# Performance work log

Measured on AMD Instinct MI355X. Metric: run time of the kernel, lower is better.

Reference implementation:

```python
import jax, jax.numpy as jnp
import numpy as np

# ---- configuration (matches init_kwargs) ----
B, C_IO, T = 2, 64, 4096
PATCH = 2
W0, W1 = 512, 1024           # widths
D_DN, D_MID = 2, 4           # depths per level
DH = 64                      # dim per head
WIN = 128                    # local attention window
MAP = 1024                   # mapping_dim
DFF_MAP = 1024               # mapping_d_ff
FF_MULT = 2                  # GEGLU ff_mult in local levels
H_DN = W0 // DH              # 8 heads
H_MID = W1 // DH             # 16 heads


def _n(key, shape, s=0.02):
    return jax.random.normal(key, shape, jnp.float32) * s


def setup_inputs() -> dict:
    key = jax.random.key(0)
    ks = iter(jax.random.split(key, 64))
    p = {}
    p['x'] = jax.random.normal(next(ks), (B, C_IO, T), jnp.float32)
    p['t'] = jax.random.uniform(next(ks), (B,), jnp.float32)
    p['time_w'] = jax.random.normal(next(ks), (MAP // 2, 1), jnp.float32)
    p['time_in_w'] = _n(next(ks), (MAP, MAP))
    p['map_in_s'] = jnp.ones((MAP,), jnp.float32)
    p['map_norm_s'] = jnp.ones((2, MAP), jnp.float32)
    p['map_up_w'] = _n(next(ks), (2, MAP, 2 * DFF_MAP))
    p['map_down_w'] = _n(next(ks), (2, DFF_MAP, MAP))
    p['map_out_s'] = jnp.ones((MAP,), jnp.float32)
    p['patch_in_w'] = _n(next(ks), (C_IO * PATCH, W0))
    p['dn_anorm_w'] = _n(next(ks), (D_DN, MAP, W0))
    p['dn_qkv_w'] = _n(next(ks), (D_DN, W0, 3 * W0))
    p['dn_o_w'] = _n(next(ks), (D_DN, W0, W0))
    p['dn_fnorm_w'] = _n(next(ks), (D_DN, MAP, W0))
    p['dn_ff1_w'] = _n(next(ks), (D_DN, W0, 2 * FF_MULT * W0))
    p['dn_ff2_w'] = _n(next(ks), (D_DN, FF_MULT * W0, W0))
    p['merge_w'] = _n(next(ks), (W0 * 2, W1))
    p['mid_map_w'] = _n(next(ks), (MAP, W1))
    p['mid_pin_w'] = _n(next(ks), (W1, W1))
    p['mid_pout_w'] = _n(next(ks), (W1, W1))
    p['mid_ln1_g'] = jnp.ones((D_MID, W1), jnp.float32)
    p['mid_ln1_b'] = jnp.zeros((D_MID, W1), jnp.float32)
    p['mid_qkv_w'] = _n(next(ks), (D_MID, W1, 3 * W1))
    p['mid_o_w'] = _n(next(ks), (D_MID, W1, W1))
    p['mid_ln2_g'] = jnp.ones((D_MID, W1), jnp.float32)
    p['mid_ln2_b'] = jnp.zeros((D_MID, W1), jnp.float32)
    p['mid_ff1_w'] = _n(next(ks), (D_MID, W1, 8 * W1))
    p['mid_ff2_w'] = _n(next(ks), (D_MID, 4 * W1, W1))
    p['mid_fn_g'] = jnp.ones((W1,), jnp.float32)
    p['mid_fn_b'] = jnp.zeros((W1,), jnp.float32)
    p['split_w'] = _n(next(ks), (W1, W0 * 2))
    p['split_fac'] = jnp.full((1,), 0.5, jnp.float32)
    p['up_anorm_w'] = _n(next(ks), (D_DN, MAP, W0))
    p['up_qkv_w'] = _n(next(ks), (D_DN, W0, 3 * W0))
    p['up_o_w'] = _n(next(ks), (D_DN, W0, W0))
    p['up_fnorm_w'] = _n(next(ks), (D_DN, MAP, W0))
    p['up_ff1_w'] = _n(next(ks), (D_DN, W0, 2 * FF_MULT * W0))
    p['up_ff2_w'] = _n(next(ks), (D_DN, FF_MULT * W0, W0))
    p['out_norm_s'] = jnp.ones((W0,), jnp.float32)
    p['patch_out_w'] = _n(next(ks), (W0, C_IO * PATCH))
    return p


def rmsnorm(x, scale, eps=1e-6):
    ms = jnp.mean(jnp.square(x), -1, keepdims=True)
    return x * (scale * jax.lax.rsqrt(ms + eps))


def layernorm(x, g, b, eps=1e-5):
    m = jnp.mean(x, -1, keepdims=True)
    v = jnp.mean(jnp.square(x - m), -1, keepdims=True)
    return (x - m) * jax.lax.rsqrt(v + eps) * g + b


def rope_tables(S, D):
    inv = 1.0 / (10000.0 ** (jnp.arange(0, D, 2, dtype=jnp.float32) / D))
    ang = jnp.arange(S, dtype=jnp.float32)[:, None] * inv  # [S, D/2]
    return jnp.cos(ang), jnp.sin(ang)


def apply_rope(x, cos, sin):
    # x: [B,H,S,D], contiguous-half rotation
    x1, x2 = jnp.split(x, 2, -1)
    return jnp.concatenate([x1 * cos - x2 * sin, x2 * cos + x1 * sin], -1)


def heads_split(x, h):
    Bx, S, C = x.shape
    return x.reshape(Bx, S, h, C // h).transpose(0, 2, 1, 3)


def heads_merge(x):
    Bx, h, S, D = x.shape
    return x.transpose(0, 2, 1, 3).reshape(Bx, S, h * D)


def local_attn(q, k, v, w):
    # non-causal sliding-window attention: each query window attends to
    # [prev, self, next] windows (look_backward=1, look_forward=1)
    Bx, H, S, D = q.shape
    nw = S // w
    qw = q.reshape(Bx, H, nw, w, D)
    def ctx(tn):
        tw = tn.reshape(Bx, H, nw, w, D)
        pad = jnp.pad(tw, ((0, 0), (0, 0), (1, 1), (0, 0), (0, 0)))
        return jnp.concatenate([pad[:, :, :-2], pad[:, :, 1:-1], pad[:, :, 2:]], 3)  # [B,H,nw,3w,D]
    kw, vw = ctx(k), ctx(v)
    s = jnp.einsum('bhnqd,bhnkd->bhnqk', qw * (D ** -0.5), kw)
    valid = jnp.ones((nw, 3 * w), bool).at[0, :w].set(False).at[-1, 2 * w:].set(False)
    s = jnp.where(valid[None, None, :, None, :], s, jnp.finfo(s.dtype).min)
    a = jax.nn.softmax(s, -1)
    return jnp.einsum('bhnqk,bhnkd->bhnqd', a, vw).reshape(Bx, H, S, D)


def token_merge(x, w, r=2):
    # 'b (n r) c -> b n (c r)' then linear
    Bx, S, C = x.shape
    x = x.reshape(Bx, S // r, r, C).transpose(0, 1, 3, 2).reshape(Bx, S // r, C * r)
    return x @ w


def token_split(x, w, r=2):
    # linear then 'b n (c r) -> b (n r) c'
    y = x @ w
    Bx, n, CR = y.shape
    C = CR // r
    return y.reshape(Bx, n, C, r).transpose(0, 1, 3, 2).reshape(Bx, n * r, C)


def mapping(e, in_s, norm_s, up_w, down_w, out_s):
    x = rmsnorm(e, in_s)
    for l in range(up_w.shape[0]):
        h = rmsnorm(x, norm_s[l])
        a, g = jnp.split(h @ up_w[l], 2, -1)
        x = x + (a * jax.nn.gelu(g)) @ down_w[l]
    return rmsnorm(x, out_s)


def local_level(x, cond, anorm, qkv_w, o_w, fnorm, ff1, ff2, heads, win):
    Bx, S, C = x.shape
    D = C // heads
    cos, sin = rope_tables(S, D)
    for l in range(qkv_w.shape[0]):
        h = rmsnorm(x, 1.0 + (cond @ anorm[l])[:, None, :])  # AdaRMSNorm
        q, k, v = jnp.split(h @ qkv_w[l], 3, -1)
        q, k, v = heads_split(q, heads), heads_split(k, heads), heads_split(v, heads)
        q, k = apply_rope(q, cos, sin), apply_rope(k, cos, sin)
        x = x + heads_merge(local_attn(q, k, v, win)) @ o_w[l]
        h = rmsnorm(x, 1.0 + (cond @ fnorm[l])[:, None, :])
        a, g = jnp.split(h @ ff1[l], 2, -1)
        x = x + (a * jax.nn.gelu(g)) @ ff2[l]  # GEGLU FF
    return x


def mid_level(x, ln1g, ln1b, qkv_w, o_w, ln2g, ln2b, ff1, ff2, fng, fnb, heads):
    Bx, S, C = x.shape
    D = C // heads
    cos, sin = rope_tables(S, D)
    for l in range(qkv_w.shape[0]):
        h = layernorm(x, ln1g[l], ln1b[l])
        q, k, v = jnp.split(h @ qkv_w[l], 3, -1)
        q, k, v = heads_split(q, heads), heads_split(k, heads), heads_split(v, heads)
        q, k = apply_rope(q, cos, sin), apply_rope(k, cos, sin)
        s = jnp.einsum('bhqd,bhkd->bhqk', q * (D ** -0.5), k)
        o = jnp.einsum('bhqk,bhkd->bhqd', jax.nn.softmax(s, -1), v)
        x = x + heads_merge(o) @ o_w[l]
        h = layernorm(x, ln2g[l], ln2b[l])
        a, g = jnp.split(h @ ff1[l], 2, -1)
        x = x + (a * jax.nn.silu(g)) @ ff2[l]  # SwiGLU FF
    return layernorm(x, fng, fnb)


def _forward(x, t, time_w, time_in_w, map_in_s, map_norm_s, map_up_w, map_down_w, map_out_s,
             patch_in_w, dn_anorm_w, dn_qkv_w, dn_o_w, dn_fnorm_w, dn_ff1_w, dn_ff2_w,
             merge_w, mid_map_w, mid_pin_w, mid_pout_w, mid_ln1_g, mid_ln1_b, mid_qkv_w,
             mid_o_w, mid_ln2_g, mid_ln2_b, mid_ff1_w, mid_ff2_w, mid_fn_g, mid_fn_b,
             split_w, split_fac, up_anorm_w, up_qkv_w, up_o_w, up_fnorm_w, up_ff1_w,
             up_ff2_w, out_norm_s, patch_out_w):
    h = jnp.swapaxes(x, 1, 2)                      # [B,T,C_io]
    h = token_merge(h, patch_in_w, PATCH)          # [B, T/2, W0]
    f = 2.0 * jnp.pi * (t[:, None] @ time_w.T)     # Fourier features
    temb = jnp.concatenate([jnp.cos(f), jnp.sin(f)], -1) @ time_in_w
    cond = mapping(temb, map_in_s, map_norm_s, map_up_w, map_down_w, map_out_s)  # [B,MAP]
    h = local_level(h, cond, dn_anorm_w, dn_qkv_w, dn_o_w, dn_fnorm_w, dn_ff1_w, dn_ff2_w, H_DN, WIN)
    skip = h
    h = token_merge(h, merge_w)                    # [B, T/4, W1]
    h = h @ mid_pin_w
    pre = (cond @ mid_map_w)[:, None, :]           # prepended mapping token
    h = jnp.concatenate([pre, h], 1)
    h = mid_level(h, mid_ln1_g, mid_ln1_b, mid_qkv_w, mid_o_w, mid_ln2_g, mid_ln2_b,
                  mid_ff1_w, mid_ff2_w, mid_fn_g, mid_fn_b, H_MID)
    h = (h @ mid_pout_w)[:, 1:, :]
    h = token_split(h, split_w)                    # back to [B, T/2, W0]
    h = skip + split_fac * (h - skip)              # lerp skip fusion
    h = local_level(h, cond, up_anorm_w, up_qkv_w, up_o_w, up_fnorm_w, up_ff1_w, up_ff2_w, H_DN, WIN)
    h = rmsnorm(h, out_norm_s)
    h = token_split(h, patch_out_w, PATCH)         # [B,T,C_io]
    return jnp.swapaxes(h, 1, 2)


def reference(x, t, time_w, time_in_w, map_in_s, map_norm_s, map_up_w, map_down_w, map_out_s,
              patch_in_w, dn_anorm_w, dn_qkv_w, dn_o_w, dn_fnorm_w, dn_ff1_w, dn_ff2_w,
              merge_w, mid_map_w, mid_pin_w, mid_pout_w, mid_ln1_g, mid_ln1_b, mid_qkv_w,
              mid_o_w, mid_ln2_g, mid_ln2_b, mid_ff1_w, mid_ff2_w, mid_fn_g, mid_fn_b,
              split_w, split_fac, up_anorm_w, up_qkv_w, up_o_w, up_fnorm_w, up_ff1_w,
              up_ff2_w, out_norm_s, patch_out_w):
    return _forward(x, t, time_w, time_in_w, map_in_s, map_norm_s, map_up_w, map_down_w, map_out_s,
                    patch_in_w, dn_anorm_w, dn_qkv_w, dn_o_w, dn_fnorm_w, dn_ff1_w, dn_ff2_w,
                    merge_w, mid_map_w, mid_pin_w, mid_pout_w, mid_ln1_g, mid_ln1_b, mid_qkv_w,
                    mid_o_w, mid_ln2_g, mid_ln2_b, mid_ff1_w, mid_ff2_w, mid_fn_g, mid_fn_b,
                    split_w, split_fac, up_anorm_w, up_qkv_w, up_o_w, up_fnorm_w, up_ff1_w,
                    up_ff2_w, out_norm_s, patch_out_w)
```

## Files before the change

kernel.cpp:

```cpp
#include <hip/hip_runtime.h>
#include <math.h>

#define BB   2
#define CIO  64
#define TT   4096
#define S0   2048
#define W0   512
#define HDN  8
#define SM   1025
#define SMP  1088
#define W1   1024
#define HMID 16
#define WIN  128
#define NW   16
#define MAPD 1024
#define KSPL 16
#define PKCAP 8396800L

typedef _Float16 f16;
typedef _Float16 half8 __attribute__((ext_vector_type(8)));
typedef _Float16 half4v __attribute__((ext_vector_type(4)));
typedef _Float16 half2v __attribute__((ext_vector_type(2)));
typedef float floatx4 __attribute__((ext_vector_type(4)));

__device__ __forceinline__ float gelu_tanh(float x) {
    float x3 = x * x * x;
    return 0.5f * x * (1.f + tanhf(0.7978845608028654f * (x + 0.044715f * x3)));
}

__global__ __launch_bounds__(256) void wcast(
    const float* __restrict__ W, f16* __restrict__ Wt, int K, int N) {
    __shared__ float T[64][65];
    const int n0 = blockIdx.x * 64, k0 = blockIdx.y * 64;
    const int tid = threadIdx.x;
    for (int e = tid; e < 4096; e += 256) {
        int r = e >> 6, c = e & 63;
        T[r][c] = W[(size_t)(k0 + r) * N + n0 + c];
    }
    __syncthreads();
    for (int e = tid; e < 2048; e += 256) {
        int r = e >> 5, c2 = (e & 31) * 2;
        half2v p;
        p[0] = (f16)T[c2][r];
        p[1] = (f16)T[c2 + 1][r];
        *(half2v*)(Wt + (size_t)(n0 + r) * K + k0 + c2) = p;
    }
}

template<int OUTM>
__global__ __launch_bounds__(256) void gemm_h(
    const f16* __restrict__ A, const f16* __restrict__ Bt,
    const float* __restrict__ res, void* __restrict__ Cv,
    int M, int N, int K) {
    __shared__ __align__(16) f16 As[2][4096];
    __shared__ __align__(16) f16 Bs[2][4096];
    const int tid = threadIdx.x;
    const int wv = tid >> 6, ln = tid & 63;
    int nwg = gridDim.x * gridDim.y;
    int orig = blockIdx.y * gridDim.x + blockIdx.x;
    int wg = orig;
    if (nwg >= 16) {
        int q = nwg >> 3, r = nwg & 7;
        int xcd = orig & 7, lot = orig >> 3;
        wg = (xcd < r ? xcd * (q + 1) : r * (q + 1) + (xcd - r) * q) + lot;
    }
    const int bm = (wg / gridDim.x) * 128, bn = (wg % gridDim.x) * 128;
    int Kc = K, kbase = 0;
    if (OUTM == 2) { Kc = K / gridDim.z; kbase = blockIdx.z * Kc; }
    const int nt = Kc >> 5;

    auto stage = [&](int buf, int kt) {
        int k0 = kbase + (kt << 5);
#pragma unroll
        for (int i = 0; i < 2; ++i) {
            int off = i * 4096 + wv * 1024 + ln * 16;
            int row = off >> 6, kb = (off & 63) >> 1;
            int gr = bm + row; gr = gr < M ? gr : M - 1;
            f16* gp = const_cast<f16*>(A) + (size_t)gr * K + k0 + kb;
            __builtin_amdgcn_global_load_lds(
                (__attribute__((address_space(1))) void*)gp,
                (__attribute__((address_space(3))) void*)(&As[buf][i * 2048 + wv * 512]),
                16, 0, 0);
            f16* gq = const_cast<f16*>(Bt) + (size_t)(bn + row) * K + k0 + kb;
            __builtin_amdgcn_global_load_lds(
                (__attribute__((address_space(1))) void*)gq,
                (__attribute__((address_space(3))) void*)(&Bs[buf][i * 2048 + wv * 512]),
                16, 0, 0);
        }
    };

    floatx4 acc[4][4];
#pragma unroll
    for (int m = 0; m < 4; ++m)
#pragma unroll
        for (int n = 0; n < 4; ++n) acc[m][n] = (floatx4)0.f;
    const int r = ln & 15, kc = (ln >> 4) * 8;
    const int wr = (wv >> 1) * 64, wc = (wv & 1) * 64;

    stage(0, 0);
    for (int t = 0; t < nt; ++t) {
        __syncthreads();
        if (t + 1 < nt) stage((t + 1) & 1, t + 1);
        const int buf = t & 1;
        half8 af[4], bf[4];
#pragma unroll
        for (int m = 0; m < 4; ++m)
            af[m] = *(const half8*)(&As[buf][(wr + m * 16 + r) * 32 + kc]);
#pragma unroll
        for (int n = 0; n < 4; ++n)
            bf[n] = *(const half8*)(&Bs[buf][(wc + n * 16 + r) * 32 + kc]);
#pragma unroll
        for (int m = 0; m < 4; ++m)
#pragma unroll
            for (int n = 0; n < 4; ++n)
                acc[m][n] = __builtin_amdgcn_mfma_f32_16x16x32_f16(af[m], bf[n], acc[m][n], 0, 0, 0);
    }

    float* Cf = (float*)Cv;
    f16*   Ch = (f16*)Cv;
    if (OUTM == 2) Cf += (size_t)blockIdx.z * M * N;
#pragma unroll
    for (int m = 0; m < 4; ++m) {
        int rbase = bm + wr + m * 16 + ((ln >> 4) << 2);
#pragma unroll
        for (int j = 0; j < 4; ++j) {
            int row = rbase + j;
            if (row < M) {
                size_t ro = (size_t)row * N;
#pragma unroll
                for (int n = 0; n < 4; ++n) {
                    int col = bn + wc + n * 16 + (ln & 15);
                    float v = acc[m][n][j];
                    if (OUTM == 1) Ch[ro + col] = (f16)v;
                    else if (OUTM == 0) Cf[ro + col] = v + (res ? res[ro + col] : 0.f);
                    else Cf[ro + col] = v;
                }
            }
        }
    }
}

template<bool HOUT>
__global__ __launch_bounds__(256) void kred(
    const float* __restrict__ P, const float* __restrict__ res,
    void* __restrict__ Cv, size_t mn, int ks) {
    size_t i = ((size_t)blockIdx.x * 256 + threadIdx.x) * 4;
    if (i >= mn) return;
    floatx4 s = res ? *(const floatx4*)(res + i) : (floatx4)0.f;
    for (int z = 0; z < ks; ++z) {
        floatx4 p = *(const floatx4*)(P + (size_t)z * mn + i);
        s += p;
    }
    if (HOUT) {
        half4v h;
#pragma unroll
        for (int j = 0; j < 4; ++j) h[j] = (f16)s[j];
        *(half4v*)((f16*)Cv + i) = h;
    } else {
        *(floatx4*)((float*)Cv + i) = s;
    }
}

__global__ __launch_bounds__(256) void gemv2_part(
    const float* __restrict__ A, const float* __restrict__ W,
    float* __restrict__ P, int N, int K) {
    int n = blockIdx.x * 256 + threadIdx.x;
    if (n >= N) return;
    int Kc = K / KSPL;
    int k0 = blockIdx.y * Kc;
    float acc0 = 0.f, acc1 = 0.f;
    const float* Wp = W + (size_t)k0 * N + n;
    const float* a0 = A + k0;
    const float* a1 = A + K + k0;
#pragma unroll 4
    for (int k = 0; k < Kc; ++k) {
        float w = Wp[(size_t)k * N];
        acc0 = fmaf(a0[k], w, acc0);
        acc1 = fmaf(a1[k], w, acc1);
    }
    P[((size_t)blockIdx.y * 2 + 0) * N + n] = acc0;
    P[((size_t)blockIdx.y * 2 + 1) * N + n] = acc1;
}

__global__ __launch_bounds__(256) void gemv2_red(
    const float* __restrict__ P, const float* __restrict__ res,
    float* __restrict__ C, int N) {
    int g = blockIdx.x * 256 + threadIdx.x;
    if (g >= 2 * N) return;
    int m = g / N, n = g - m * N;
    float s = res ? res[g] : 0.f;
#pragma unroll
    for (int ky = 0; ky < KSPL; ++ky)
        s += P[((size_t)ky * 2 + m) * N + n];
    C[g] = s;
}

__device__ __forceinline__ void stf(float* p, float v) { *p = v; }
__device__ __forceinline__ void stf(f16* p, float v)   { *p = (f16)v; }

template<typename TO>
__global__ __launch_bounds__(256) void rmsnorm_k(
    const float* __restrict__ X, const float* __restrict__ scale,
    TO* __restrict__ Y, int C, int rows_per_group, float sadd) {
    int row = blockIdx.x, tid = threadIdx.x;
    const float* x = X + (size_t)row * C;
    float v[8];
    int cnt = C >> 8;
    float ss = 0.f;
    for (int i = 0; i < cnt; ++i) { v[i] = x[tid + (i << 8)]; ss += v[i] * v[i]; }
    __shared__ float red[256];
    red[tid] = ss; __syncthreads();
    for (int s2 = 128; s2; s2 >>= 1) { if (tid < s2) red[tid] += red[tid + s2]; __syncthreads(); }
    float inv = rsqrtf(red[0] / (float)C + 1e-6f);
    const float* sc = scale + (size_t)(row / rows_per_group) * C;
    TO* y = Y + (size_t)row * C;
    for (int i = 0; i < cnt; ++i) {
        int c = tid + (i << 8);
        stf(&y[c], v[i] * (sadd + sc[c]) * inv);
    }
}

__global__ __launch_bounds__(256) void layernorm_k(
    const float* __restrict__ X, const float* __restrict__ g,
    const float* __restrict__ bta, f16* __restrict__ Y, int C) {
    int row = blockIdx.x, tid = threadIdx.x;
    const float* x = X + (size_t)row * C;
    float v[8];
    int cnt = C >> 8;
    float s = 0.f;
    for (int i = 0; i < cnt; ++i) { v[i] = x[tid + (i << 8)]; s += v[i]; }
    __shared__ float red[256];
    red[tid] = s; __syncthreads();
    for (int s2 = 128; s2; s2 >>= 1) { if (tid < s2) red[tid] += red[tid + s2]; __syncthreads(); }
    float m = red[0] / (float)C;
    __syncthreads();
    float s2s = 0.f;
    for (int i = 0; i < cnt; ++i) { float d = v[i] - m; s2s += d * d; }
    red[tid] = s2s; __syncthreads();
    for (int s2 = 128; s2; s2 >>= 1) { if (tid < s2) red[tid] += red[tid + s2]; __syncthreads(); }
    float inv = rsqrtf(red[0] / (float)C + 1e-5f);
    f16* y = Y + (size_t)row * C;
    for (int i = 0; i < cnt; ++i) {
        int c = tid + (i << 8);
        y[c] = (f16)((v[i] - m) * inv * g[c] + bta[c]);
    }
}

__global__ __launch_bounds__(256) void glu_k(
    const float* __restrict__ U, float* __restrict__ Yo,
    size_t total, int F, int mode) {
    size_t gidx = (size_t)blockIdx.x * 256 + threadIdx.x;
    if (gidx >= total) return;
    size_t r = gidx / (size_t)F;
    int c = (int)(gidx - r * F);
    const float* u = U + r * (size_t)(2 * F);
    float a = u[c], gg = u[F + c];
    float act = (mode == 0) ? gelu_tanh(gg) : gg / (1.f + expf(-gg));
    Yo[gidx] = a * act;
}

__global__ __launch_bounds__(256) void glu_h8(
    const f16* __restrict__ U, f16* __restrict__ Yo,
    size_t total8, int F8, int mode) {
    size_t gi = (size_t)blockIdx.x * 256 + threadIdx.x;
    if (gi >= total8) return;
    size_t r = gi / (size_t)F8;
    int c = (int)(gi - r * (size_t)F8);
    const f16* u = U + r * (size_t)F8 * 16;
    half8 av = *(const half8*)(u + c * 8);
    half8 gv = *(const half8*)(u + F8 * 8 + c * 8);
    half8 y;
#pragma unroll
    for (int j = 0; j < 8; ++j) {
        float a = (float)av[j], gg = (float)gv[j];
        float act = (mode == 0) ? gelu_tanh(gg) : gg / (1.f + __expf(-gg));
        y[j] = (f16)(a * act);
    }
    *(half8*)(Yo + gi * 8) = y;
}

__global__ __launch_bounds__(256) void qkv_split_rope(
    const float* __restrict__ QKV, f16* __restrict__ Qo,
    f16* __restrict__ Ko, f16* __restrict__ Vo, int S, int H) {
    int g = blockIdx.x * 256 + threadIdx.x;
    int total = BB * S * H * 32;
    if (g >= total) return;
    int i = g & 31;
    int tix = g >> 5;
    int h = tix % H; tix /= H;
    int s = tix % S; int b = tix / S;
    int C = H * 64;
    const float* base = QKV + (size_t)(b * S + s) * 3 * C + h * 64;
    float q1 = base[i], q2 = base[32 + i];
    float k1 = base[C + i], k2 = base[C + 32 + i];
    float v1 = base[2 * C + i], v2 = base[2 * C + 32 + i];
    float inv = expf(-(float)i * 0.28782313662425575f);
    float ang = (float)s * inv;
    float sn, cs;
    sincosf(ang, &sn, &cs);
    size_t o = ((size_t)(b * H + h) * S + s) * 64 + i;
    Qo[o]      = (f16)((q1 * cs - q2 * sn) * 0.125f);
    Qo[o + 32] = (f16)((q2 * cs + q1 * sn) * 0.125f);
    Ko[o]      = (f16)(k1 * cs - k2 * sn);
    Ko[o + 32] = (f16)(k2 * cs + k1 * sn);
    Vo[o]      = (f16)v1;
    Vo[o + 32] = (f16)v2;
}

__global__ __launch_bounds__(256) void vtrans(
    const f16* __restrict__ V, f16* __restrict__ Vt, int S, int Spad) {
    __shared__ f16 T[64][72];
    const int tid = threadIdx.x;
    const int k0 = blockIdx.x * 64;
    const f16* Vb = V + (size_t)blockIdx.y * S * 64;
    f16* Vtb = Vt + (size_t)blockIdx.y * 64 * Spad;
    for (int c = tid; c < 512; c += 256) {
        int kk = c >> 3, d8 = (c & 7) * 8;
        int kg = k0 + kk; kg = kg < S ? kg : S - 1;
        half8 v = *(const half8*)(Vb + (size_t)kg * 64 + d8);
        if (k0 + kk >= S) {
#pragma unroll
            for (int j = 0; j < 8; ++j) v[j] = (f16)0.f;
        }
        *(half8*)(&T[kk][d8]) = v;
    }
    __syncthreads();
    for (int c = tid; c < 512; c += 256) {
        int d = c >> 3, k8 = (c & 7) * 8;
        half8 o;
#pragma unroll
        for (int j = 0; j < 8; ++j) o[j] = T[k8 + j][d];
        *(half8*)(Vtb + (size_t)d * Spad + k0 + k8) = o;
    }
}

__global__ __launch_bounds__(256) void fattn(
    const f16* __restrict__ Q, const f16* __restrict__ K,
    const f16* __restrict__ Vt, f16* __restrict__ O,
    int S, int Spad, int H, int win) {
    __shared__ __align__(16) f16 Ks[64][72];
    __shared__ __align__(16) f16 Vs[64][72];
    __shared__ __align__(16) f16 Ps[4][32][72];
    const int tid = threadIdx.x;
    const int wv = tid >> 6, ln = tid & 63;
    const int r15 = ln & 15, g = ln >> 4;
    const int bh = blockIdx.y;
    const int b = bh / H, h = bh % H;
    const int q0 = (int)blockIdx.x * 128;
    const f16* Qb = Q + (size_t)bh * S * 64;
    const f16* Kb = K + (size_t)bh * S * 64;
    const f16* Vtb = Vt + (size_t)bh * 64 * Spad;

    half8 aq[2][2];
#pragma unroll
    for (int m = 0; m < 2; ++m) {
        int q = q0 + wv * 32 + m * 16 + r15;
        q = q < S ? q : S - 1;
#pragma unroll
        for (int ks = 0; ks < 2; ++ks)
            aq[m][ks] = *(const half8*)(Qb + (size_t)q * 64 + ks * 32 + g * 8);
    }
    floatx4 o[2][4];
#pragma unroll
    for (int m = 0; m < 2; ++m)
#pragma unroll
        for (int n = 0; n < 4; ++n) o[m][n] = (floatx4)0.f;
    float mst[2][4], lst[2][4];
#pragma unroll
    for (int m = 0; m < 2; ++m)
#pragma unroll
        for (int j = 0; j < 4; ++j) { mst[m][j] = -3.0e38f; lst[m][j] = 0.f; }

    int klo = 0, khi = S;
    if (win) {
        int n = (int)blockIdx.x;
        klo = (n - 1) * win; if (klo < 0) klo = 0;
        khi = (n + 2) * win; if (khi > S) khi = S;
    }
    for (int kb = klo; kb < khi; kb += 64) {
        __syncthreads();
#pragma unroll
        for (int i = 0; i < 2; ++i) {
            int c = tid + i * 256;
            int rr = c >> 3, c8 = (c & 7) * 8;
            int kg = kb + rr; kg = kg < S ? kg : S - 1;
            *(half8*)(&Ks[rr][c8]) = *(const half8*)(Kb + (size_t)kg * 64 + c8);
            *(half8*)(&Vs[rr][c8]) = *(const half8*)(Vtb + (size_t)rr * Spad + kb + c8);
        }
        __syncthreads();
        floatx4 s[2][4];
#pragma unroll
        for (int m = 0; m < 2; ++m)
#pragma unroll
            for (int n = 0; n < 4; ++n) s[m][n] = (floatx4)0.f;
#pragma unroll
        for (int ks = 0; ks < 2; ++ks) {
            half8 bk[4];
#pragma unroll
            for (int n = 0; n < 4; ++n)
                bk[n] = *(const half8*)(&Ks[n * 16 + r15][ks * 32 + g * 8]);
#pragma unroll
            for (int m = 0; m < 2; ++m)
#pragma unroll
                for (int n = 0; n < 4; ++n)
                    s[m][n] = __builtin_amdgcn_mfma_f32_16x16x32_f16(aq[m][ks], bk[n], s[m][n], 0, 0, 0);
        }
        if (kb + 64 > S) {
#pragma unroll
            for (int n = 0; n < 4; ++n)
                if (kb + n * 16 + r15 >= S) {
#pragma unroll
                    for (int m = 0; m < 2; ++m) s[m][n] = (floatx4)(-3.0e38f);
                }
        }
#pragma unroll
        for (int m = 0; m < 2; ++m) {
#pragma unroll
            for (int j = 0; j < 4; ++j) {
                float tm = fmaxf(fmaxf(s[m][0][j], s[m][1][j]), fmaxf(s[m][2][j], s[m][3][j]));
                tm = fmaxf(tm, __shfl_xor(tm, 1));
                tm = fmaxf(tm, __shfl_xor(tm, 2));
                tm = fmaxf(tm, __shfl_xor(tm, 4));
                tm = fmaxf(tm, __shfl_xor(tm, 8));
                float mn = fmaxf(mst[m][j], tm);
                float sc = __expf(mst[m][j] - mn);
                mst[m][j] = mn;
                float ts = 0.f;
#pragma unroll
                for (int n = 0; n < 4; ++n) {
                    float p = __expf(s[m][n][j] - mn);
                    s[m][n][j] = p;
                    ts += p;
                }
                ts += __shfl_xor(ts, 1);
                ts += __shfl_xor(ts, 2);
                ts += __shfl_xor(ts, 4);
                ts += __shfl_xor(ts, 8);
                lst[m][j] = lst[m][j] * sc + ts;
#pragma unroll
                for (int n = 0; n < 4; ++n) o[m][n][j] *= sc;
            }
        }
#pragma unroll
        for (int m = 0; m < 2; ++m)
#pragma unroll
            for (int n = 0; n < 4; ++n)
#pragma unroll
                for (int j = 0; j < 4; ++j)
                    Ps[wv][m * 16 + g * 4 + j][n * 16 + r15] = (f16)s[m][n][j];
#pragma unroll
        for (int ks = 0; ks < 2; ++ks) {
            half8 pa[2], bv[4];
#pragma unroll
            for (int m = 0; m < 2; ++m)
                pa[m] = *(const half8*)(&Ps[wv][m * 16 + r15][ks * 32 + g * 8]);
#pragma unroll
            for (int n = 0; n < 4; ++n)
                bv[n] = *(const half8*)(&Vs[n * 16 + r15][ks * 32 + g * 8]);
#pragma unroll
            for (int m = 0; m < 2; ++m)
#pragma unroll
                for (int n = 0; n < 4; ++n)
                    o[m][n] = __builtin_amdgcn_mfma_f32_16x16x32_f16(pa[m], bv[n], o[m][n], 0, 0, 0);
        }
    }
    const int HC = H * 64;
#pragma unroll
    for (int m = 0; m < 2; ++m)
#pragma unroll
        for (int j = 0; j < 4; ++j) {
            int q = q0 + wv * 32 + m * 16 + g * 4 + j;
            if (q < S) {
                float inv = 1.f / lst[m][j];
                size_t ro = ((size_t)b * S + q) * HC + h * 64;
#pragma unroll
                for (int n = 0; n < 4; ++n)
                    O[ro + n * 16 + r15] = (f16)(o[m][n][j] * inv);
            }
        }
}

__global__ __launch_bounds__(256) void patch_in_gather(
    const float* __restrict__ x, f16* __restrict__ out) {
    int g = blockIdx.x * 256 + threadIdx.x;
    if (g >= BB * S0 * 128) return;
    int k = g & 127;
    int n = (g >> 7) & (S0 - 1);
    int b = g >> 18;
    out[g] = (f16)x[(size_t)b * CIO * TT + (size_t)(k >> 1) * TT + 2 * n + (k & 1)];
}

__global__ __launch_bounds__(256) void time_embed(
    const float* __restrict__ t, const float* __restrict__ tw,
    float* __restrict__ te) {
    int g = blockIdx.x * 256 + threadIdx.x;
    if (g >= BB * MAPD) return;
    int b = g / MAPD, j = g % MAPD;
    float w = tw[(j < 512) ? j : j - 512];
    float ang = 6.283185307179586f * t[b] * w;
    te[g] = (j < 512) ? cosf(ang) : sinf(ang);
}

__global__ __launch_bounds__(256) void token_merge_gather(
    const float* __restrict__ A, f16* __restrict__ out) {
    int g = blockIdx.x * 256 + threadIdx.x;
    if (g >= BB * 1024 * 1024) return;
    int k = g & 1023;
    int n = (g >> 10) & 1023;
    int b = g >> 20;
    out[g] = (f16)A[((size_t)b * S0 + 2 * n + (k & 1)) * W0 + (k >> 1)];
}

__global__ __launch_bounds__(256) void concat_mid(
    const float* __restrict__ pre, const float* __restrict__ Dsrc,
    float* __restrict__ Cm) {
    int g = blockIdx.x * 256 + threadIdx.x;
    if (g >= BB * SM * W1) return;
    int c = g & 1023;
    int row = g >> 10;
    int b = row / SM, r = row % SM;
    Cm[g] = (r == 0) ? pre[b * W1 + c]
                     : Dsrc[((size_t)b * 1024 + r - 1) * W1 + c];
}

__global__ __launch_bounds__(256) void gather_drop(
    const f16* __restrict__ Dsrc, f16* __restrict__ out) {
    int g = blockIdx.x * 256 + threadIdx.x;
    if (g >= BB * 1024 * W1) return;
    int c = g & 1023;
    int n = (g >> 10) & 1023;
    int b = g >> 20;
    out[g] = Dsrc[((size_t)b * SM + 1 + n) * W1 + c];
}

__global__ __launch_bounds__(256) void split_scatter_lerp(
    const float* __restrict__ y, const float* __restrict__ skip,
    const float* __restrict__ fac, float* __restrict__ xo) {
    int g = blockIdx.x * 256 + threadIdx.x;
    if (g >= BB * S0 * W0) return;
    int c = g & 511;
    int tk = (g >> 9) & (S0 - 1);
    int b = g >> 20;
    float yv = y[((size_t)b * 1024 + (tk >> 1)) * W1 + (c * 2 + (tk & 1))];
    float sk = skip[g];
    xo[g] = sk + fac[0] * (yv - sk);
}

__global__ __launch_bounds__(256) void patch_out_scatter(
    const float* __restrict__ y, float* __restrict__ out) {
    int g = blockIdx.x * 256 + threadIdx.x;
    if (g >= BB * CIO * TT) return;
    int tk = g & (TT - 1);
    int c = (g >> 12) & 63;
    int b = g >> 18;
    out[g] = y[((size_t)b * S0 + (tk >> 1)) * 128 + (c * 2 + (tk & 1))];
}

extern "C" void kernel_launch(void* const* d_in, const int* in_sizes, int n_in,
                              void* d_out, int out_size, void* d_ws, size_t ws_size,
                              hipStream_t stream) {
    const float* x          = (const float*)d_in[0];
    const float* t          = (const float*)d_in[1];
    const float* time_w     = (const float*)d_in[2];
    const float* time_in_w  = (const float*)d_in[3];
    const float* map_in_s   = (const float*)d_in[4];
    const float* map_norm_s = (const float*)d_in[5];
    const float* map_up_w   = (const float*)d_in[6];
    const float* map_down_w = (const float*)d_in[7];
    const float* map_out_s  = (const float*)d_in[8];
    const float* patch_in_w = (const float*)d_in[9];
    const float* dn_anorm_w = (const float*)d_in[10];
    const float* dn_qkv_w   = (const float*)d_in[11];
    const float* dn_o_w     = (const float*)d_in[12];
    const float* dn_fnorm_w = (const float*)d_in[13];
    const float* dn_ff1_w   = (const float*)d_in[14];
    const float* dn_ff2_w   = (const float*)d_in[15];
    const float* merge_w    = (const float*)d_in[16];
    const float* mid_map_w  = (const float*)d_in[17];
    const float* mid_pin_w  = (const float*)d_in[18];
    const float* mid_pout_w = (const float*)d_in[19];
    const float* mid_ln1_g  = (const float*)d_in[20];
    const float* mid_ln1_b  = (const float*)d_in[21];
    const float* mid_qkv_w  = (const float*)d_in[22];
    const float* mid_o_w    = (const float*)d_in[23];
    const float* mid_ln2_g  = (const float*)d_in[24];
    const float* mid_ln2_b  = (const float*)d_in[25];
    const float* mid_ff1_w  = (const float*)d_in[26];
    const float* mid_ff2_w  = (const float*)d_in[27];
    const float* mid_fn_g   = (const float*)d_in[28];
    const float* mid_fn_b   = (const float*)d_in[29];
    const float* split_w    = (const float*)d_in[30];
    const float* split_fac  = (const float*)d_in[31];
    const float* up_anorm_w = (const float*)d_in[32];
    const float* up_qkv_w   = (const float*)d_in[33];
    const float* up_o_w     = (const float*)d_in[34];
    const float* up_fnorm_w = (const float*)d_in[35];
    const float* up_ff1_w   = (const float*)d_in[36];
    const float* up_ff2_w   = (const float*)d_in[37];
    const float* out_norm_s = (const float*)d_in[38];
    const float* patch_out_w= (const float*)d_in[39];

    float* Wp = (float*)d_ws;
    size_t off = 0;
    auto alloc = [&](size_t n) { float* p = Wp + off; off += n; return p; };
    float* A   = alloc((size_t)4096 * 512);
    float* Bsk = alloc((size_t)4096 * 512);
    float* Cm  = alloc((size_t)2050 * 1024);
    float* Df  = alloc((size_t)2050 * 1024);
    float* E32 = alloc((size_t)2050 * 3072);
    f16*  Fq   = (f16*)alloc((size_t)1049600);
    f16*  Fk   = (f16*)alloc((size_t)1049600);
    f16*  Fv   = (f16*)alloc((size_t)1049600);
    f16*  Fvt  = (f16*)alloc((size_t)1114112);
    f16*  H1   = (f16*)alloc((size_t)8396800);
    f16*  H2   = (f16*)alloc((size_t)4198400);
    f16*  Wh   = (f16*)alloc((size_t)4194304);
    float* Pk  = alloc((size_t)PKCAP);
    float* Pb  = alloc((size_t)KSPL * 2 * 2048);
    float* Sma = alloc((size_t)32768);
    (void)ws_size; (void)in_sizes; (void)n_in; (void)out_size;

    float* te   = Sma;
    float* temb = Sma + 2048;
    float* mapx = Sma + 4096;
    float* maph = Sma + 6144;
    float* mapu = Sma + 8192;
    float* mapg = Sma + 12288;
    float* cond = Sma + 14336;
    float* sA   = Sma + 16384;
    float* sF   = Sma + 17408;
    float* pre  = Sma + 18432;

    auto WC = [&](const float* W, int K, int N) {
        wcast<<<dim3(N / 64, K / 64), 256, 0, stream>>>(W, Wh, K, N);
    };
    auto pick_ks = [](int M, int N, int K) {
        long gx = N / 128, gy = (M + 127) / 128;
        int ks = 1;
        while (gx * gy * ks < 512 && ks < 8) {
            int nk = ks * 2;
            if ((K / nk) % 32 != 0 || (long)M * N * nk > PKCAP) break;
            ks = nk;
        }
        return ks;
    };
    auto GF = [&](const f16* Aa, const float* res, float* C, int M, int N, int K) {
        int ks = pick_ks(M, N, K);
        dim3 g(N / 128, (M + 127) / 128, ks);
        if (ks == 1) {
            gemm_h<0><<<g, 256, 0, stream>>>(Aa, Wh, res, C, M, N, K);
        } else {
            gemm_h<2><<<g, 256, 0, stream>>>(Aa, Wh, nullptr, Pk, M, N, K);
            size_t mn = (size_t)M * N;
            kred<false><<<(int)((mn / 4 + 255) / 256), 256, 0, stream>>>(Pk, res, C, mn, ks);
        }
    };
    auto GH = [&](const f16* Aa, f16* C, int M, int N, int K) {
        int ks = pick_ks(M, N, K);
        dim3 g(N / 128, (M + 127) / 128, ks);
        if (ks == 1) {
            gemm_h<1><<<g, 256, 0, stream>>>(Aa, Wh, nullptr, C, M, N, K);
        } else {
            gemm_h<2><<<g, 256, 0, stream>>>(Aa, Wh, nullptr, Pk, M, N, K);
            size_t mn = (size_t)M * N;
            kred<true><<<(int)((mn / 4 + 255) / 256), 256, 0, stream>>>(Pk, nullptr, C, mn, ks);
        }
    };
    auto gemv2 = [&](const float* Aa, const float* W, const float* res,
                     float* C, int N, int K) {
        gemv2_part<<<dim3((N + 255) / 256, KSPL), 256, 0, stream>>>(Aa, W, Pb, N, K);
        gemv2_red<<<(2 * N + 255) / 256, 256, 0, stream>>>(Pb, res, C, N);
    };

    patch_in_gather<<<(BB * S0 * 128 + 255) / 256, 256, 0, stream>>>(x, H2);
    WC(patch_in_w, 128, 512);
    GF(H2, nullptr, A, 4096, 512, 128);

    time_embed<<<(BB * MAPD + 255) / 256, 256, 0, stream>>>(t, time_w, te);
    gemv2(te, time_in_w, nullptr, temb, 1024, 1024);
    rmsnorm_k<float><<<2, 256, 0, stream>>>(temb, map_in_s, mapx, 1024, 2, 0.f);
    for (int l = 0; l < 2; ++l) {
        rmsnorm_k<float><<<2, 256, 0, stream>>>(mapx, map_norm_s + (size_t)l * 1024, maph, 1024, 2, 0.f);
        gemv2(maph, map_up_w + (size_t)l * 1024 * 2048, nullptr, mapu, 2048, 1024);
        glu_k<<<(2 * 1024 + 255) / 256, 256, 0, stream>>>(mapu, mapg, 2 * 1024, 1024, 0);
        gemv2(mapg, map_down_w + (size_t)l * 1024 * 1024, mapx, mapx, 1024, 1024);
    }
    rmsnorm_k<float><<<2, 256, 0, stream>>>(mapx, map_out_s, cond, 1024, 2, 0.f);

    auto run_local = [&](const float* anorm, const float* qkvw, const float* ow,
                         const float* fnorm, const float* ff1, const float* ff2) {
        for (int l = 0; l < 2; ++l) {
            gemv2(cond, anorm + (size_t)l * 1024 * 512, nullptr, sA, 512, 1024);
            rmsnorm_k<f16><<<4096, 256, 0, stream>>>(A, sA, H2, 512, 2048, 1.f);
            WC(qkvw + (size_t)l * 512 * 1536, 512, 1536);
            GF(H2, nullptr, E32, 4096, 1536, 512);
            qkv_split_rope<<<(BB * S0 * HDN * 32 + 255) / 256, 256, 0, stream>>>(E32, Fq, Fk, Fv, S0, HDN);
            vtrans<<<dim3(S0 / 64, BB * HDN), 256, 0, stream>>>(Fv, Fvt, S0, S0);
            fattn<<<dim3(S0 / 128, BB * HDN), 256, 0, stream>>>(Fq, Fk, Fvt, H2, S0, S0, HDN, WIN);
            WC(ow + (size_t)l * 512 * 512, 512, 512);
            GF(H2, A, A, 4096, 512, 512);
            gemv2(cond, fnorm + (size_t)l * 1024 * 512, nullptr, sF, 512, 1024);
            rmsnorm_k<f16><<<4096, 256, 0, stream>>>(A, sF, H2, 512, 2048, 1.f);
            WC(ff1 + (size_t)l * 512 * 2048, 512, 2048);
            GH(H2, H1, 4096, 2048, 512);
            glu_h8<<<(4096 * 128 + 255) / 256, 256, 0, stream>>>(H1, H2, (size_t)4096 * 128, 128, 0);
            WC(ff2 + (size_t)l * 1024 * 512, 1024, 512);
            GF(H2, A, A, 4096, 512, 1024);
        }
    };
    run_local(dn_anorm_w, dn_qkv_w, dn_o_w, dn_fnorm_w, dn_ff1_w, dn_ff2_w);

    hipMemcpyAsync(Bsk, A, (size_t)4096 * 512 * 4, hipMemcpyDeviceToDevice, stream);
    token_merge_gather<<<(BB * 1024 * 1024 + 255) / 256, 256, 0, stream>>>(A, H2);
    WC(merge_w, 1024, 1024);
    GH(H2, H1, 2048, 1024, 1024);
    WC(mid_pin_w, 1024, 1024);
    GF(H1, nullptr, Df, 2048, 1024, 1024);
    gemv2(cond, mid_map_w, nullptr, pre, 1024, 1024);
    concat_mid<<<(BB * SM * W1 + 255) / 256, 256, 0, stream>>>(pre, Df, Cm);

    for (int l = 0; l < 4; ++l) {
        layernorm_k<<<2050, 256, 0, stream>>>(Cm, mid_ln1_g + (size_t)l * 1024,
                                              mid_ln1_b + (size_t)l * 1024, H2, 1024);
        WC(mid_qkv_w + (size_t)l * 1024 * 3072, 1024, 3072);
        GF(H2, nullptr, E32, 2050, 3072, 1024);
        qkv_split_rope<<<(BB * SM * HMID * 32 + 255) / 256, 256, 0, stream>>>(E32, Fq, Fk, Fv, SM, HMID);
        vtrans<<<dim3(SMP / 64, BB * HMID), 256, 0, stream>>>(Fv, Fvt, SM, SMP);
        fattn<<<dim3(9, BB * HMID), 256, 0, stream>>>(Fq, Fk, Fvt, H2, SM, SMP, HMID, 0);
        WC(mid_o_w + (size_t)l * 1024 * 1024, 1024, 1024);
        GF(H2, Cm, Cm, 2050, 1024, 1024);
        layernorm_k<<<2050, 256, 0, stream>>>(Cm, mid_ln2_g + (size_t)l * 1024,
                                              mid_ln2_b + (size_t)l * 1024, H2, 1024);
        WC(mid_ff1_w + (size_t)l * 1024 * 8192, 1024, 8192);
        GH(H2, H1, 2050, 8192, 1024);
        glu_h8<<<(int)(((size_t)2050 * 512 + 255) / 256), 256, 0, stream>>>(H1, H2, (size_t)2050 * 512, 512, 1);
        WC(mid_ff2_w + (size_t)l * 4096 * 1024, 4096, 1024);
        GF(H2, Cm, Cm, 2050, 1024, 4096);
    }
    layernorm_k<<<2050, 256, 0, stream>>>(Cm, mid_fn_g, mid_fn_b, H2, 1024);

    WC(mid_pout_w, 1024, 1024);
    GH(H2, H1, 2050, 1024, 1024);
    gather_drop<<<(BB * 1024 * W1 + 255) / 256, 256, 0, stream>>>(H1, H2);
    WC(split_w, 1024, 1024);
    GF(H2, nullptr, Df, 2048, 1024, 1024);
    split_scatter_lerp<<<(BB * S0 * W0 + 255) / 256, 256, 0, stream>>>(Df, Bsk, split_fac, A);

    run_local(up_anorm_w, up_qkv_w, up_o_w, up_fnorm_w, up_ff1_w, up_ff2_w);

    rmsnorm_k<f16><<<4096, 256, 0, stream>>>(A, out_norm_s, H2, 512, 4096, 0.f);
    WC(patch_out_w, 512, 128);
    GF(H2, nullptr, Df, 4096, 128, 512);
    patch_out_scatter<<<(BB * CIO * TT + 255) / 256, 256, 0, stream>>>(Df, (float*)d_out);
}
```

Baseline: 2.187 ms.

## Split attention over key ranges with separate softmax-combine kernel

Adds a split-K (flash-decoding style) mode to the attention kernel: each block handles a slice of key tiles and writes unnormalized fp32 partial outputs plus running max and sum. A new combine kernel merges the partials with log-sum-exp weighting and writes fp16 output. The goal is more blocks in flight for the low-occupancy attention grids (9x32 mid, 16x16 local). The cost is extra fp32 partial traffic, an extra launch, and reuse of the Pk scratch buffer.

```diff
diff --git a/kernel.cpp b/kernel.cpp
--- a/kernel.cpp
+++ b/kernel.cpp
@@ -336,8 +336,9 @@
 
 __global__ __launch_bounds__(256) void fattn(
     const f16* __restrict__ Q, const f16* __restrict__ K,
-    const f16* __restrict__ Vt, f16* __restrict__ O,
-    int S, int Spad, int H, int win) {
+    const f16* __restrict__ Vt, float* __restrict__ Op,
+    float* __restrict__ Mst, float* __restrict__ Lst,
+    int S, int Spad, int H, int win, int QR) {
     __shared__ __align__(16) f16 Ks[64][72];
     __shared__ __align__(16) f16 Vs[64][72];
     __shared__ __align__(16) f16 Ps[4][32][72];
@@ -345,7 +346,8 @@
     const int wv = tid >> 6, ln = tid & 63;
     const int r15 = ln & 15, g = ln >> 4;
     const int bh = blockIdx.y;
-    const int b = bh / H, h = bh % H;
+    const int NBH = gridDim.y;
+    const int z = blockIdx.z, nz = gridDim.z;
     const int q0 = (int)blockIdx.x * 128;
     const f16* Qb = Q + (size_t)bh * S * 64;
     const f16* Kb = K + (size_t)bh * S * 64;
@@ -377,7 +379,12 @@
         klo = (n - 1) * win; if (klo < 0) klo = 0;
         khi = (n + 2) * win; if (khi > S) khi = S;
     }
-    for (int kb = klo; kb < khi; kb += 64) {
+    int ntile = (khi - klo + 63) >> 6;
+    int chunk = (ntile + nz - 1) / nz;
+    int myLo = klo + z * chunk * 64;
+    int myHi = klo + (z + 1) * chunk * 64; if (myHi > khi) myHi = khi;
+
+    for (int kb = myLo; kb < myHi; kb += 64) {
         __syncthreads();
 #pragma unroll
         for (int i = 0; i < 2; ++i) {
@@ -464,20 +471,51 @@
                     o[m][n] = __builtin_amdgcn_mfma_f32_16x16x32_f16(pa[m], bv[n], o[m][n], 0, 0, 0);
         }
     }
-    const int HC = H * 64;
+    size_t zb = ((size_t)z * NBH + bh) * QR;
 #pragma unroll
     for (int m = 0; m < 2; ++m)
 #pragma unroll
         for (int j = 0; j < 4; ++j) {
-            int q = q0 + wv * 32 + m * 16 + g * 4 + j;
-            if (q < S) {
-                float inv = 1.f / lst[m][j];
-                size_t ro = ((size_t)b * S + q) * HC + h * 64;
-#pragma unroll
-                for (int n = 0; n < 4; ++n)
-                    O[ro + n * 16 + r15] = (f16)(o[m][n][j] * inv);
+            int qr = q0 + wv * 32 + m * 16 + g * 4 + j;
+            size_t ro = (zb + qr) * 64;
+#pragma unroll
+            for (int n = 0; n < 4; ++n)
+                Op[ro + n * 16 + r15] = o[m][n][j];
+            if (r15 == 0) {
+                Mst[zb + qr] = mst[m][j];
+                Lst[zb + qr] = lst[m][j];
             }
         }
+}
+
+__global__ __launch_bounds__(256) void fcomb(
+    const float* __restrict__ Op, const float* __restrict__ Mst,
+    const float* __restrict__ Lst, f16* __restrict__ O,
+    int S, int H, int QR, int nz, int rows) {
+    int g = blockIdx.x * 256 + threadIdx.x;
+    int idx = g >> 4;
+    int d4 = (g & 15) * 4;
+    if (idx >= rows) return;
+    int bh = idx / QR, q = idx - bh * QR;
+    if (q >= S) return;
+    float mstar = -3.0e38f;
+    for (int z = 0; z < nz; ++z)
+        mstar = fmaxf(mstar, Mst[(size_t)z * rows + idx]);
+    float den = 0.f;
+    floatx4 num = (floatx4)0.f;
+    for (int z = 0; z < nz; ++z) {
+        float w = __expf(Mst[(size_t)z * rows + idx] - mstar);
+        den += w * Lst[(size_t)z * rows + idx];
+        floatx4 ov = *(const floatx4*)(Op + ((size_t)z * rows + idx) * 64 + d4);
+        num += w * ov;
+    }
+    float inv = 1.f / den;
+    int b = bh / H, h = bh % H;
+    f16* op = O + ((size_t)b * S + q) * (H * 64) + h * 64 + d4;
+    half4v hv;
+#pragma unroll
+    for (int j = 0; j < 4; ++j) hv[j] = (f16)(num[j] * inv);
+    *(half4v*)op = hv;
 }
 
 __global__ __launch_bounds__(256) void patch_in_gather(
@@ -616,6 +654,7 @@
     f16*  H2   = (f16*)alloc((size_t)4198400);
     f16*  Wh   = (f16*)alloc((size_t)4194304);
     float* Pk  = alloc((size_t)PKCAP);
+    float* ML  = alloc((size_t)262144);
     float* Pb  = alloc((size_t)KSPL * 2 * 2048);
     float* Sma = alloc((size_t)32768);
     (void)ws_size; (void)in_sizes; (void)n_in; (void)out_size;
@@ -671,6 +710,15 @@
         gemv2_part<<<dim3((N + 255) / 256, KSPL), 256, 0, stream>>>(Aa, W, Pb, N, K);
         gemv2_red<<<(2 * N + 255) / 256, 256, 0, stream>>>(Pb, res, C, N);
     };
+    auto FATT = [&](const f16* Qp, const f16* Kp, const f16* Vtp, f16* Out,
+                    int S, int Spad, int H, int win, int nq, int nbh, int nz) {
+        int QR = nq * 128;
+        int rows = nbh * QR;
+        fattn<<<dim3(nq, nbh, nz), 256, 0, stream>>>(
+            Qp, Kp, Vtp, Pk, ML, ML + (size_t)nz * rows, S, Spad, H, win, QR);
+        fcomb<<<(rows * 16 + 255) / 256, 256, 0, stream>>>(
+            Pk, ML, ML + (size_t)nz * rows, Out, S, H, QR, nz, rows);
+    };
 
     patch_in_gather<<<(BB * S0 * 128 + 255) / 256, 256, 0, stream>>>(x, H2);
     WC(patch_in_w, 128, 512);
@@ -696,7 +744,7 @@
             GF(H2, nullptr, E32, 4096, 1536, 512);
             qkv_split_rope<<<(BB * S0 * HDN * 32 + 255) / 256, 256, 0, stream>>>(E32, Fq, Fk, Fv, S0, HDN);
             vtrans<<<dim3(S0 / 64, BB * HDN), 256, 0, stream>>>(Fv, Fvt, S0, S0);
-            fattn<<<dim3(S0 / 128, BB * HDN), 256, 0, stream>>>(Fq, Fk, Fvt, H2, S0, S0, HDN, WIN);
+            FATT(Fq, Fk, Fvt, H2, S0, S0, HDN, WIN, S0 / 128, BB * HDN, 2);
             WC(ow + (size_t)l * 512 * 512, 512, 512);
             GF(H2, A, A, 4096, 512, 512);
             gemv2(cond, fnorm + (size_t)l * 1024 * 512, nullptr, sF, 512, 1024);
@@ -726,7 +774,7 @@
         GF(H2, nullptr, E32, 2050, 3072, 1024);
         qkv_split_rope<<<(BB * SM * HMID * 32 + 255) / 256, 256, 0, stream>>>(E32, Fq, Fk, Fv, SM, HMID);
         vtrans<<<dim3(SMP / 64, BB * HMID), 256, 0, stream>>>(Fv, Fvt, SM, SMP);
-        fattn<<<dim3(9, BB * HMID), 256, 0, stream>>>(Fq, Fk, Fvt, H2, SM, SMP, HMID, 0);
+        FATT(Fq, Fk, Fvt, H2, SM, SMP, HMID, 0, 9, BB * HMID, 3);
         WC(mid_o_w + (size_t)l * 1024 * 1024, 1024, 1024);
         GF(H2, Cm, Cm, 2050, 1024, 1024);
         layernorm_k<<<2050, 256, 0, stream>>>(Cm, mid_ln2_g + (size_t)l * 1024,
```

New measurement: 2.146 ms. No clear change (-1.9%).
